# Optimization experiments

Hardware: AMD Instinct MI355X
Metric: run time of the kernel (lower is better)

Reference implementation:

```python
import jax, jax.numpy as jnp
import numpy as np

N_NODES = 100000
N_EDGES = 600000
VOCAB = 50000
EMBED_DIM = 128
HIDDEN_DIM = 128


def gcn_conv(h, W, b, src, dst, n_nodes):
    """PyG GCNConv: x' = D^{-1/2} (A+I) D^{-1/2} X W + b.
    src/dst already include self-loops."""
    hw = h @ W                                   # [N, out]
    deg = jnp.zeros((n_nodes,), hw.dtype).at[dst].add(1.0)   # in-degree incl. self-loop
    dinv = jax.lax.rsqrt(deg)                    # deg >= 1 thanks to self-loops
    norm = dinv[src] * dinv[dst]                 # [E+N]
    msgs = norm[:, None] * hw[src]               # gather [E+N, out]
    out = jnp.zeros_like(hw).at[dst].add(msgs)   # scatter-aggregate
    return out + b


def setup_inputs() -> dict:
    key = jax.random.key(0)
    ks = jax.random.split(key, 8)
    x = jax.random.randint(ks[0], (N_NODES,), 0, VOCAB, dtype=jnp.int64 if jax.config.jax_enable_x64 else jnp.int32)
    edge_index = jax.random.randint(ks[1], (2, N_EDGES), 0, N_NODES, dtype=jnp.int32)
    emb = jax.random.normal(ks[2], (VOCAB, EMBED_DIM), dtype=jnp.float32)
    # Glorot-style scale for GCN weights
    W1 = jax.random.normal(ks[3], (EMBED_DIM, HIDDEN_DIM), dtype=jnp.float32) * (1.0 / np.sqrt(EMBED_DIM))
    b1 = jnp.zeros((HIDDEN_DIM,), dtype=jnp.float32)
    W2 = jax.random.normal(ks[4], (HIDDEN_DIM, HIDDEN_DIM), dtype=jnp.float32) * (1.0 / np.sqrt(HIDDEN_DIM))
    b2 = jnp.zeros((HIDDEN_DIM,), dtype=jnp.float32)
    return {"x": x, "edge_index": edge_index, "emb": emb, "W1": W1, "b1": b1, "W2": W2, "b2": b2}


def reference(x, edge_index, emb, W1, b1, W2, b2):
    n = x.shape[0]
    loops = jnp.arange(n, dtype=edge_index.dtype)
    src = jnp.concatenate([edge_index[0], loops])  # add self-loops once
    dst = jnp.concatenate([edge_index[1], loops])
    h = emb[x]                                     # [N, embed_dim] embedding lookup
    h = jax.nn.relu(gcn_conv(h, W1, b1, src, dst, n))
    h = jax.nn.relu(gcn_conv(h, W2, b2, src, dst, n))
    return h
```

## Files before the change

kernel.cpp:

```cpp
#include <hip/hip_runtime.h>
#include <hip/hip_fp16.h>


#define NDIM 128
#define PAD_K 136
#define SCAN_IPT 4
#define SCAN_BLK 256
#define SCAN_IPB (SCAN_BLK * SCAN_IPT)

typedef __bf16 bf16x8 __attribute__((ext_vector_type(8)));
typedef float f32x4 __attribute__((ext_vector_type(4)));

__device__ __forceinline__ float bf2f(unsigned short u) {
    union { unsigned int i; float f; } c;
    c.i = (unsigned int)u << 16;
    return c.f;
}
__device__ __forceinline__ unsigned short f2bf(float f) {
    __bf16 b = (__bf16)f;
    return __builtin_bit_cast(unsigned short, b);
}
__device__ __forceinline__ unsigned short f2h(float f) {
    __half h = __float2half_rn(f);
    return __builtin_bit_cast(unsigned short, h);
}
__device__ __forceinline__ float h2f(unsigned short u) {
    return __half2float(__builtin_bit_cast(__half, u));
}
__device__ __forceinline__ void unpack8(uint4 q, float* f) {
    f[0] = bf2f((unsigned short)(q.x & 0xffff));
    f[1] = bf2f((unsigned short)(q.x >> 16));
    f[2] = bf2f((unsigned short)(q.y & 0xffff));
    f[3] = bf2f((unsigned short)(q.y >> 16));
    f[4] = bf2f((unsigned short)(q.z & 0xffff));
    f[5] = bf2f((unsigned short)(q.z >> 16));
    f[6] = bf2f((unsigned short)(q.w & 0xffff));
    f[7] = bf2f((unsigned short)(q.w >> 16));
}

__global__ void degree_count(const int* __restrict__ dst, int* __restrict__ cnt, int E) {
    const int stride = gridDim.x * blockDim.x;
    int e = blockIdx.x * blockDim.x + threadIdx.x;
#pragma unroll
    for (int k = 0; k < 4; ++k) {
        int ee = e + k * stride;
        if (ee < E) atomicAdd(&cnt[dst[ee]], 1);
    }
}

__global__ void scan_blocks(const int* __restrict__ in, int* __restrict__ out,
                            int* __restrict__ bsums, int n) {
    __shared__ int lds[SCAN_BLK];
    const int t = threadIdx.x;
    const int base = blockIdx.x * SCAN_IPB + t * SCAN_IPT;
    int v[SCAN_IPT];
    int s = 0;
#pragma unroll
    for (int k = 0; k < SCAN_IPT; ++k) { v[k] = (base + k < n) ? in[base + k] : 0; s += v[k]; }
    lds[t] = s;
    __syncthreads();
    for (int off = 1; off < SCAN_BLK; off <<= 1) {
        int x = (t >= off) ? lds[t - off] : 0;
        __syncthreads();
        lds[t] += x;
        __syncthreads();
    }
    if (t == SCAN_BLK - 1) bsums[blockIdx.x] = lds[t];
    int run = (t == 0) ? 0 : lds[t - 1];
#pragma unroll
    for (int k = 0; k < SCAN_IPT; ++k) {
        if (base + k < n) out[base + k] = run;
        run += v[k];
    }
}

__global__ void scan_partials(int* __restrict__ bsums, int nb) {
    __shared__ int lds[128];
    const int t = threadIdx.x;
    lds[t] = (t < nb) ? bsums[t] : 0;
    __syncthreads();
    for (int off = 1; off < 128; off <<= 1) {
        int x = (t >= off) ? lds[t - off] : 0;
        __syncthreads();
        lds[t] += x;
        __syncthreads();
    }
    if (t < nb) bsums[t] = (t == 0) ? 0 : lds[t - 1];
}

__global__ void add_offsets_dinv_wt(int* __restrict__ rp, const int* __restrict__ bsums,
                                    const int* __restrict__ cnt, float* __restrict__ dinv, int n,
                                    int nblkA,
                                    const float* __restrict__ W1, const float* __restrict__ W2,
                                    unsigned short* __restrict__ WT1,
                                    unsigned short* __restrict__ WT2) {
    if ((int)blockIdx.x < nblkA) {
        int i = blockIdx.x * blockDim.x + threadIdx.x;
        if (i < n) {
            rp[i] += bsums[i / SCAN_IPB];
            dinv[i] = rsqrtf((float)cnt[i] + 1.0f);
        }
    } else {
        int c = (blockIdx.x - nblkA) * blockDim.x + threadIdx.x;
        int cc = c & 16383;
        int j = cc >> 7, k = cc & 127;
        if (c < 16384) WT1[cc] = f2bf(W1[k * 128 + j]);
        else if (c < 32768) WT2[cc] = f2bf(W2[k * 128 + j]);
    }
}

__global__ void fill_edges(const int* __restrict__ src, const int* __restrict__ dst,
                           int* __restrict__ rp, const int* __restrict__ x,
                           const float* __restrict__ dinv, int2* __restrict__ ew, int E) {
    const int stride = gridDim.x * blockDim.x;
    const int e0 = blockIdx.x * blockDim.x + threadIdx.x;
    int s[4], d[4];
#pragma unroll
    for (int k = 0; k < 4; ++k) {
        int ee = e0 + k * stride;
        if (ee < E) { s[k] = src[ee]; d[k] = dst[ee]; } else { s[k] = -1; }
    }
    int xs[4];
    float ds[4];
#pragma unroll
    for (int k = 0; k < 4; ++k) {
        if (s[k] >= 0) { xs[k] = x[s[k]]; ds[k] = dinv[s[k]]; }
    }
#pragma unroll
    for (int k = 0; k < 4; ++k) {
        if (s[k] >= 0) {
            int p = atomicAdd(&rp[d[k]], 1);
            ew[p] = make_int2(s[k], (int)(((unsigned)f2h(ds[k]) << 16) | (unsigned)xs[k]));
        }
    }
}

template <int MODE, bool SCALE>
__global__ __launch_bounds__(256, 4)
void gemm_mfma(const void* __restrict__ Asrc, const unsigned short* __restrict__ WTb,
               const float* __restrict__ dinv, unsigned short* __restrict__ outb, int n) {
    __shared__ __bf16 sBT[128 * PAD_K];
    const int tid = threadIdx.x;
    const int rbase = blockIdx.x * 64;

    {
        const uint4* bsrc = (const uint4*)WTb;
#pragma unroll
        for (int i = 0; i < 8; ++i) {
            int c = tid + i * 256;
            int j = c >> 4, u = c & 15;
            *(uint4*)&sBT[j * PAD_K + u * 8] = bsrc[c];
        }
    }
    __syncthreads();

    const int wave = tid >> 6, lane = tid & 63;
    const int quad = lane >> 4, lrow = lane & 15;
    int arow = rbase + wave * 16 + lrow;
    if (arow >= n) arow = n - 1;

    f32x4 acc[8];
#pragma unroll
    for (int nt = 0; nt < 8; ++nt) acc[nt] = (f32x4)0.0f;

#pragma unroll
    for (int ks = 0; ks < 4; ++ks) {
        const int kb = ks * 32 + quad * 8;
        bf16x8 a;
        if (MODE == 0) {
            const float4* A4 = (const float4*)Asrc;
            float4 v0 = A4[(size_t)arow * 32 + (kb >> 2)];
            float4 v1 = A4[(size_t)arow * 32 + (kb >> 2) + 1];
            a = (bf16x8){(__bf16)v0.x, (__bf16)v0.y, (__bf16)v0.z, (__bf16)v0.w,
                         (__bf16)v1.x, (__bf16)v1.y, (__bf16)v1.z, (__bf16)v1.w};
        } else {
            a = *(const bf16x8*)((const unsigned short*)Asrc + (size_t)arow * 128 + kb);
        }
#pragma unroll
        for (int nt = 0; nt < 8; ++nt) {
            bf16x8 b = *(const bf16x8*)&sBT[(nt * 16 + lrow) * PAD_K + kb];
            acc[nt] = __builtin_amdgcn_mfma_f32_16x16x32_bf16(a, b, acc[nt], 0, 0, 0);
        }
    }

#pragma unroll
    for (int r = 0; r < 4; ++r) {
        int grow = rbase + wave * 16 + quad * 4 + r;
        if (grow < n) {
            float dsc = SCALE ? dinv[grow] : 1.0f;
            unsigned short* orow = outb + (size_t)grow * NDIM + lrow;
#pragma unroll
            for (int nt = 0; nt < 8; ++nt)
                orow[nt * 16] = f2bf(SCALE ? dsc * acc[nt][r] : acc[nt][r]);
        }
    }
}

__global__ void aggregate1(const unsigned short* __restrict__ tab, const int* __restrict__ x,
                           const int* __restrict__ rp, const int2* __restrict__ ew,
                           const float* __restrict__ dinv, const float* __restrict__ bias,
                           unsigned short* __restrict__ outb, int n, int half) {
    int t = blockIdx.x * blockDim.x + threadIdx.x;
    int g = t >> 4, u = t & 15;
    if (g >= half) return;
    const uint4* tab4 = (const uint4*)tab;
    const int i0 = g, i1 = g + half;
    const bool has1 = (i1 < n);
    float di0 = dinv[i0];
    float di1 = has1 ? dinv[i1] : 0.0f;
    float acc0[8], acc1[8];
    {
        float f[8];
        unpack8(tab4[(size_t)x[i0] * 16 + u], f);
#pragma unroll
        for (int k = 0; k < 8; ++k) acc0[k] = di0 * f[k];
    }
    if (has1) {
        float f[8];
        unpack8(tab4[(size_t)x[i1] * 16 + u], f);
#pragma unroll
        for (int k = 0; k < 8; ++k) acc1[k] = di1 * f[k];
    }
    int j0 = (i0 == 0) ? 0 : rp[i0 - 1];
    const int e0 = rp[i0];
    int j1 = has1 ? rp[i1 - 1] : 0;
    const int e1 = has1 ? rp[i1] : 0;

    while (j0 + 2 <= e0 && j1 + 2 <= e1) {
        int2 a0 = ew[j0], a1 = ew[j0 + 1], c0 = ew[j1], c1 = ew[j1 + 1];
        uint4 qa0 = tab4[(size_t)(a0.y & 0xffff) * 16 + u];
        uint4 qa1 = tab4[(size_t)(a1.y & 0xffff) * 16 + u];
        uint4 qc0 = tab4[(size_t)(c0.y & 0xffff) * 16 + u];
        uint4 qc1 = tab4[(size_t)(c1.y & 0xffff) * 16 + u];
        float fa0[8], fa1[8], fc0[8], fc1[8];
        unpack8(qa0, fa0); unpack8(qa1, fa1); unpack8(qc0, fc0); unpack8(qc1, fc1);
        float na0 = h2f((unsigned short)((unsigned)a0.y >> 16));
        float na1 = h2f((unsigned short)((unsigned)a1.y >> 16));
        float nc0 = h2f((unsigned short)((unsigned)c0.y >> 16));
        float nc1 = h2f((unsigned short)((unsigned)c1.y >> 16));
#pragma unroll
        for (int k = 0; k < 8; ++k) {
            acc0[k] += fmaf(na0, fa0[k], na1 * fa1[k]);
            acc1[k] += fmaf(nc0, fc0[k], nc1 * fc1[k]);
        }
        j0 += 2; j1 += 2;
    }
    for (; j0 + 2 <= e0; j0 += 2) {
        int2 a0 = ew[j0], a1 = ew[j0 + 1];
        uint4 qa0 = tab4[(size_t)(a0.y & 0xffff) * 16 + u];
        uint4 qa1 = tab4[(size_t)(a1.y & 0xffff) * 16 + u];
        float fa0[8], fa1[8];
        unpack8(qa0, fa0); unpack8(qa1, fa1);
        float na0 = h2f((unsigned short)((unsigned)a0.y >> 16));
        float na1 = h2f((unsigned short)((unsigned)a1.y >> 16));
#pragma unroll
        for (int k = 0; k < 8; ++k) acc0[k] += fmaf(na0, fa0[k], na1 * fa1[k]);
    }
    if (j0 < e0) {
        int2 a = ew[j0];
        uint4 q = tab4[(size_t)(a.y & 0xffff) * 16 + u];
        float f[8];
        unpack8(q, f);
        float nm = h2f((unsigned short)((unsigned)a.y >> 16));
#pragma unroll
        for (int k = 0; k < 8; ++k) acc0[k] = fmaf(nm, f[k], acc0[k]);
    }
    for (; j1 + 2 <= e1; j1 += 2) {
        int2 c0 = ew[j1], c1 = ew[j1 + 1];
        uint4 qc0 = tab4[(size_t)(c0.y & 0xffff) * 16 + u];
        uint4 qc1 = tab4[(size_t)(c1.y & 0xffff) * 16 + u];
        float fc0[8], fc1[8];
        unpack8(qc0, fc0); unpack8(qc1, fc1);
        float nc0 = h2f((unsigned short)((unsigned)c0.y >> 16));
        float nc1 = h2f((unsigned short)((unsigned)c1.y >> 16));
#pragma unroll
        for (int k = 0; k < 8; ++k) acc1[k] += fmaf(nc0, fc0[k], nc1 * fc1[k]);
    }
    if (j1 < e1) {
        int2 c = ew[j1];
        uint4 q = tab4[(size_t)(c.y & 0xffff) * 16 + u];
        float f[8];
        unpack8(q, f);
        float nm = h2f((unsigned short)((unsigned)c.y >> 16));
#pragma unroll
        for (int k = 0; k < 8; ++k) acc1[k] = fmaf(nm, f[k], acc1[k]);
    }

    const float4 b0 = ((const float4*)bias)[u * 2];
    const float4 b1 = ((const float4*)bias)[u * 2 + 1];
    {
        float r[8];
        r[0] = fmaxf(fmaf(di0, acc0[0], b0.x), 0.0f);
        r[1] = fmaxf(fmaf(di0, acc0[1], b0.y), 0.0f);
        r[2] = fmaxf(fmaf(di0, acc0[2], b0.z), 0.0f);
        r[3] = fmaxf(fmaf(di0, acc0[3], b0.w), 0.0f);
        r[4] = fmaxf(fmaf(di0, acc0[4], b1.x), 0.0f);
        r[5] = fmaxf(fmaf(di0, acc0[5], b1.y), 0.0f);
        r[6] = fmaxf(fmaf(di0, acc0[6], b1.z), 0.0f);
        r[7] = fmaxf(fmaf(di0, acc0[7], b1.w), 0.0f);
        uint4 o;
        o.x = (unsigned)f2bf(r[0]) | ((unsigned)f2bf(r[1]) << 16);
        o.y = (unsigned)f2bf(r[2]) | ((unsigned)f2bf(r[3]) << 16);
        o.z = (unsigned)f2bf(r[4]) | ((unsigned)f2bf(r[5]) << 16);
        o.w = (unsigned)f2bf(r[6]) | ((unsigned)f2bf(r[7]) << 16);
        ((uint4*)outb)[(size_t)i0 * 16 + u] = o;
    }
    if (has1) {
        float r[8];
        r[0] = fmaxf(fmaf(di1, acc1[0], b0.x), 0.0f);
        r[1] = fmaxf(fmaf(di1, acc1[1], b0.y), 0.0f);
        r[2] = fmaxf(fmaf(di1, acc1[2], b0.z), 0.0f);
        r[3] = fmaxf(fmaf(di1, acc1[3], b0.w), 0.0f);
        r[4] = fmaxf(fmaf(di1, acc1[4], b1.x), 0.0f);
        r[5] = fmaxf(fmaf(di1, acc1[5], b1.y), 0.0f);
        r[6] = fmaxf(fmaf(di1, acc1[6], b1.z), 0.0f);
        r[7] = fmaxf(fmaf(di1, acc1[7], b1.w), 0.0f);
        uint4 o;
        o.x = (unsigned)f2bf(r[0]) | ((unsigned)f2bf(r[1]) << 16);
        o.y = (unsigned)f2bf(r[2]) | ((unsigned)f2bf(r[3]) << 16);
        o.z = (unsigned)f2bf(r[4]) | ((unsigned)f2bf(r[5]) << 16);
        o.w = (unsigned)f2bf(r[6]) | ((unsigned)f2bf(r[7]) << 16);
        ((uint4*)outb)[(size_t)i1 * 16 + u] = o;
    }
}

__global__ void aggregate2(const unsigned short* __restrict__ vs, const int* __restrict__ rp,
                           const int2* __restrict__ ew, const float* __restrict__ dinv,
                           const float* __restrict__ bias, float* __restrict__ out,
                           int n, int half) {
    int t = blockIdx.x * blockDim.x + threadIdx.x;
    int g = t >> 4, u = t & 15;
    if (g >= half) return;
    const uint4* vs4 = (const uint4*)vs;
    const int i0 = g, i1 = g + half;
    const bool has1 = (i1 < n);
    float acc0[8], acc1[8];
    unpack8(vs4[(size_t)i0 * 16 + u], acc0);
    if (has1) unpack8(vs4[(size_t)i1 * 16 + u], acc1);
    int j0 = (i0 == 0) ? 0 : rp[i0 - 1];
    const int e0 = rp[i0];
    int j1 = has1 ? rp[i1 - 1] : 0;
    const int e1 = has1 ? rp[i1] : 0;

    while (j0 + 2 <= e0 && j1 + 2 <= e1) {
        int s00 = ew[j0].x, s01 = ew[j0 + 1].x, s10 = ew[j1].x, s11 = ew[j1 + 1].x;
        uint4 q00 = vs4[(size_t)s00 * 16 + u];
        uint4 q01 = vs4[(size_t)s01 * 16 + u];
        uint4 q10 = vs4[(size_t)s10 * 16 + u];
        uint4 q11 = vs4[(size_t)s11 * 16 + u];
        float f00[8], f01[8], f10[8], f11[8];
        unpack8(q00, f00); unpack8(q01, f01); unpack8(q10, f10); unpack8(q11, f11);
#pragma unroll
        for (int k = 0; k < 8; ++k) {
            acc0[k] += f00[k] + f01[k];
            acc1[k] += f10[k] + f11[k];
        }
        j0 += 2; j1 += 2;
    }
    for (; j0 + 2 <= e0; j0 += 2) {
        int s00 = ew[j0].x, s01 = ew[j0 + 1].x;
        uint4 q00 = vs4[(size_t)s00 * 16 + u];
        uint4 q01 = vs4[(size_t)s01 * 16 + u];
        float f00[8], f01[8];
        unpack8(q00, f00); unpack8(q01, f01);
#pragma unroll
        for (int k = 0; k < 8; ++k) acc0[k] += f00[k] + f01[k];
    }
    if (j0 < e0) {
        uint4 q = vs4[(size_t)ew[j0].x * 16 + u];
        float f[8];
        unpack8(q, f);
#pragma unroll
        for (int k = 0; k < 8; ++k) acc0[k] += f[k];
    }
    for (; j1 + 2 <= e1; j1 += 2) {
        int s10 = ew[j1].x, s11 = ew[j1 + 1].x;
        uint4 q10 = vs4[(size_t)s10 * 16 + u];
        uint4 q11 = vs4[(size_t)s11 * 16 + u];
        float f10[8], f11[8];
        unpack8(q10, f10); unpack8(q11, f11);
#pragma unroll
        for (int k = 0; k < 8; ++k) acc1[k] += f10[k] + f11[k];
    }
    if (j1 < e1) {
        uint4 q = vs4[(size_t)ew[j1].x * 16 + u];
        float f[8];
        unpack8(q, f);
#pragma unroll
        for (int k = 0; k < 8; ++k) acc1[k] += f[k];
    }

    const float4 b0 = ((const float4*)bias)[u * 2];
    const float4 b1 = ((const float4*)bias)[u * 2 + 1];
    {
        float di = dinv[i0];
        float4 r0, r1;
        r0.x = fmaxf(fmaf(di, acc0[0], b0.x), 0.0f);
        r0.y = fmaxf(fmaf(di, acc0[1], b0.y), 0.0f);
        r0.z = fmaxf(fmaf(di, acc0[2], b0.z), 0.0f);
        r0.w = fmaxf(fmaf(di, acc0[3], b0.w), 0.0f);
        r1.x = fmaxf(fmaf(di, acc0[4], b1.x), 0.0f);
        r1.y = fmaxf(fmaf(di, acc0[5], b1.y), 0.0f);
        r1.z = fmaxf(fmaf(di, acc0[6], b1.z), 0.0f);
        r1.w = fmaxf(fmaf(di, acc0[7], b1.w), 0.0f);
        ((float4*)out)[(size_t)i0 * 32 + u * 2] = r0;
        ((float4*)out)[(size_t)i0 * 32 + u * 2 + 1] = r1;
    }
    if (has1) {
        float di = dinv[i1];
        float4 r0, r1;
        r0.x = fmaxf(fmaf(di, acc1[0], b0.x), 0.0f);
        r0.y = fmaxf(fmaf(di, acc1[1], b0.y), 0.0f);
        r0.z = fmaxf(fmaf(di, acc1[2], b0.z), 0.0f);
        r0.w = fmaxf(fmaf(di, acc1[3], b0.w), 0.0f);
        r1.x = fmaxf(fmaf(di, acc1[4], b1.x), 0.0f);
        r1.y = fmaxf(fmaf(di, acc1[5], b1.y), 0.0f);
        r1.z = fmaxf(fmaf(di, acc1[6], b1.z), 0.0f);
        r1.w = fmaxf(fmaf(di, acc1[7], b1.w), 0.0f);
        ((float4*)out)[(size_t)i1 * 32 + u * 2] = r0;
        ((float4*)out)[(size_t)i1 * 32 + u * 2 + 1] = r1;
    }
}

extern "C" void kernel_launch(void* const* d_in, const int* in_sizes, int n_in,
                              void* d_out, int out_size, void* d_ws, size_t ws_size,
                              hipStream_t stream) {
    const int* x = (const int*)d_in[0];
    const int* edge_index = (const int*)d_in[1];
    const float* emb = (const float*)d_in[2];
    const float* W1 = (const float*)d_in[3];
    const float* b1 = (const float*)d_in[4];
    const float* W2 = (const float*)d_in[5];
    const float* b2 = (const float*)d_in[6];
    float* out = (float*)d_out;

    const int N = in_sizes[0];
    const int E = in_sizes[1] / 2;
    const int V = in_sizes[2] / NDIM;
    const int* src = edge_index;
    const int* dst = edge_index + E;

    char* p = (char*)d_ws;
    auto alloc = [&](size_t bytes) {
        char* q = p;
        p += (bytes + 511) & ~(size_t)511;
        return q;
    };
    int* cnt = (int*)alloc((size_t)N * sizeof(int));
    int* rp = (int*)alloc((size_t)N * sizeof(int));
    float* dinv = (float*)alloc((size_t)N * sizeof(float));
    int* bsums = (int*)alloc(128 * sizeof(int));
    int2* ew = (int2*)alloc((size_t)E * sizeof(int2));
    unsigned short* WT1 = (unsigned short*)alloc(16384 * sizeof(unsigned short));
    unsigned short* WT2 = (unsigned short*)alloc(16384 * sizeof(unsigned short));
    unsigned short* embW1 = (unsigned short*)alloc((size_t)V * NDIM * sizeof(unsigned short));
    unsigned short* h1b = (unsigned short*)alloc((size_t)N * NDIM * sizeof(unsigned short));
    unsigned short* vs2 = (unsigned short*)alloc((size_t)N * NDIM * sizeof(unsigned short));
    (void)ws_size;

    const int NB = (N + SCAN_IPB - 1) / SCAN_IPB;
    const int nblkA = (N + 255) / 256;
    const int half = (N + 1) / 2;

    hipMemsetAsync(cnt, 0, (size_t)N * sizeof(int), stream);
    degree_count<<<(E / 4 + 255) / 256, 256, 0, stream>>>(dst, cnt, E);
    scan_blocks<<<NB, SCAN_BLK, 0, stream>>>(cnt, rp, bsums, N);
    scan_partials<<<1, 128, 0, stream>>>(bsums, NB);
    add_offsets_dinv_wt<<<nblkA + 128, 256, 0, stream>>>(rp, bsums, cnt, dinv, N, nblkA,
                                                         W1, W2, WT1, WT2);
    fill_edges<<<(E / 4 + 255) / 256, 256, 0, stream>>>(src, dst, rp, x, dinv, ew, E);

    const int agg_blocks = (int)(((size_t)half * 16 + 255) / 256);

    gemm_mfma<0, false><<<(V + 63) / 64, 256, 0, stream>>>(emb, WT1, nullptr, embW1, V);
    aggregate1<<<agg_blocks, 256, 0, stream>>>(embW1, x, rp, ew, dinv, b1, h1b, N, half);
    gemm_mfma<1, true><<<(N + 63) / 64, 256, 0, stream>>>(h1b, WT2, dinv, vs2, N);
    aggregate2<<<agg_blocks, 256, 0, stream>>>(vs2, rp, ew, dinv, b2, out, N, half);
}
```

Measured before the change: 251.8 us.

## Merge embedding GEMM and CSR edge fill into one launch

The embedding-table GEMM and the edge fill that builds the CSR are combined into a single heterogeneous kernel. Block index decides whether a block runs the MFMA GEMM or the fill. This lets the two independent stages run concurrently and removes one launch. Degree counting and the fill now process 2 edges per thread instead of 4, giving more blocks with less work each. The fill blocks carry the GEMM's shared-memory allocation and launch bounds, which may limit their occupancy.

```diff
diff --git a/kernel.cpp b/kernel.cpp
--- a/kernel.cpp
+++ b/kernel.cpp
@@ -42,7 +42,7 @@
     const int stride = gridDim.x * blockDim.x;
     int e = blockIdx.x * blockDim.x + threadIdx.x;
 #pragma unroll
-    for (int k = 0; k < 4; ++k) {
+    for (int k = 0; k < 2; ++k) {
         int ee = e + k * stride;
         if (ee < E) atomicAdd(&cnt[dst[ee]], 1);
     }
@@ -109,36 +109,83 @@
     }
 }
 
-__global__ void fill_edges(const int* __restrict__ src, const int* __restrict__ dst,
-                           int* __restrict__ rp, const int* __restrict__ x,
-                           const float* __restrict__ dinv, int2* __restrict__ ew, int E) {
-    const int stride = gridDim.x * blockDim.x;
-    const int e0 = blockIdx.x * blockDim.x + threadIdx.x;
-    int s[4], d[4];
-#pragma unroll
-    for (int k = 0; k < 4; ++k) {
-        int ee = e0 + k * stride;
-        if (ee < E) { s[k] = src[ee]; d[k] = dst[ee]; } else { s[k] = -1; }
-    }
-    int xs[4];
-    float ds[4];
-#pragma unroll
-    for (int k = 0; k < 4; ++k) {
-        if (s[k] >= 0) { xs[k] = x[s[k]]; ds[k] = dinv[s[k]]; }
-    }
-#pragma unroll
-    for (int k = 0; k < 4; ++k) {
-        if (s[k] >= 0) {
-            int p = atomicAdd(&rp[d[k]], 1);
-            ew[p] = make_int2(s[k], (int)(((unsigned)f2h(ds[k]) << 16) | (unsigned)xs[k]));
-        }
-    }
-}
-
-template <int MODE, bool SCALE>
 __global__ __launch_bounds__(256, 4)
-void gemm_mfma(const void* __restrict__ Asrc, const unsigned short* __restrict__ WTb,
-               const float* __restrict__ dinv, unsigned short* __restrict__ outb, int n) {
+void gemm1_fill(const float* __restrict__ emb, const unsigned short* __restrict__ WT1,
+                unsigned short* __restrict__ embW1, int V, int gemmBlocks,
+                const int* __restrict__ src, const int* __restrict__ dst,
+                int* __restrict__ rp, const int* __restrict__ x,
+                const float* __restrict__ dinv, int2* __restrict__ ew, int E,
+                int fillBlocks) {
+    __shared__ __bf16 sBT[128 * PAD_K];
+    const int tid = threadIdx.x;
+
+    if ((int)blockIdx.x < gemmBlocks) {
+        const int rbase = blockIdx.x * 64;
+        {
+            const uint4* bsrc = (const uint4*)WT1;
+#pragma unroll
+            for (int i = 0; i < 8; ++i) {
+                int c = tid + i * 256;
+                int j = c >> 4, u = c & 15;
+                *(uint4*)&sBT[j * PAD_K + u * 8] = bsrc[c];
+            }
+        }
+        __syncthreads();
+
+        const int wave = tid >> 6, lane = tid & 63;
+        const int quad = lane >> 4, lrow = lane & 15;
+        int arow = rbase + wave * 16 + lrow;
+        if (arow >= V) arow = V - 1;
+
+        f32x4 acc[8];
+#pragma unroll
+        for (int nt = 0; nt < 8; ++nt) acc[nt] = (f32x4)0.0f;
+
+#pragma unroll
+        for (int ks = 0; ks < 4; ++ks) {
+            const int kb = ks * 32 + quad * 8;
+            const float4* A4 = (const float4*)emb;
+            float4 v0 = A4[(size_t)arow * 32 + (kb >> 2)];
+            float4 v1 = A4[(size_t)arow * 32 + (kb >> 2) + 1];
+            bf16x8 a = (bf16x8){(__bf16)v0.x, (__bf16)v0.y, (__bf16)v0.z, (__bf16)v0.w,
+                                (__bf16)v1.x, (__bf16)v1.y, (__bf16)v1.z, (__bf16)v1.w};
+#pragma unroll
+            for (int nt = 0; nt < 8; ++nt) {
+                bf16x8 b = *(const bf16x8*)&sBT[(nt * 16 + lrow) * PAD_K + kb];
+                acc[nt] = __builtin_amdgcn_mfma_f32_16x16x32_bf16(a, b, acc[nt], 0, 0, 0);
+            }
+        }
+
+#pragma unroll
+        for (int r = 0; r < 4; ++r) {
+            int grow = rbase + wave * 16 + quad * 4 + r;
+            if (grow < V) {
+                unsigned short* orow = embW1 + (size_t)grow * NDIM + lrow;
+#pragma unroll
+                for (int nt = 0; nt < 8; ++nt)
+                    orow[nt * 16] = f2bf(acc[nt][r]);
+            }
+        }
+    } else {
+        const int bid = blockIdx.x - gemmBlocks;
+        const int stride = fillBlocks * 256;
+        int e = bid * 256 + tid;
+#pragma unroll
+        for (int k = 0; k < 2; ++k, e += stride) {
+            if (e < E) {
+                int d = dst[e], s = src[e];
+                int xs = x[s];
+                float ds = dinv[s];
+                int p = atomicAdd(&rp[d], 1);
+                ew[p] = make_int2(s, (int)(((unsigned)f2h(ds) << 16) | (unsigned)xs));
+            }
+        }
+    }
+}
+
+__global__ __launch_bounds__(256, 4)
+void gemm_mfma_b(const unsigned short* __restrict__ Asrc, const unsigned short* __restrict__ WTb,
+                 const float* __restrict__ dinv, unsigned short* __restrict__ outb, int n) {
     __shared__ __bf16 sBT[128 * PAD_K];
     const int tid = threadIdx.x;
     const int rbase = blockIdx.x * 64;
@@ -166,16 +213,7 @@
 #pragma unroll
     for (int ks = 0; ks < 4; ++ks) {
         const int kb = ks * 32 + quad * 8;
-        bf16x8 a;
-        if (MODE == 0) {
-            const float4* A4 = (const float4*)Asrc;
-            float4 v0 = A4[(size_t)arow * 32 + (kb >> 2)];
-            float4 v1 = A4[(size_t)arow * 32 + (kb >> 2) + 1];
-            a = (bf16x8){(__bf16)v0.x, (__bf16)v0.y, (__bf16)v0.z, (__bf16)v0.w,
-                         (__bf16)v1.x, (__bf16)v1.y, (__bf16)v1.z, (__bf16)v1.w};
-        } else {
-            a = *(const bf16x8*)((const unsigned short*)Asrc + (size_t)arow * 128 + kb);
-        }
+        bf16x8 a = *(const bf16x8*)(Asrc + (size_t)arow * 128 + kb);
 #pragma unroll
         for (int nt = 0; nt < 8; ++nt) {
             bf16x8 b = *(const bf16x8*)&sBT[(nt * 16 + lrow) * PAD_K + kb];
@@ -187,11 +225,11 @@
     for (int r = 0; r < 4; ++r) {
         int grow = rbase + wave * 16 + quad * 4 + r;
         if (grow < n) {
-            float dsc = SCALE ? dinv[grow] : 1.0f;
+            float dsc = dinv[grow];
             unsigned short* orow = outb + (size_t)grow * NDIM + lrow;
 #pragma unroll
             for (int nt = 0; nt < 8; ++nt)
-                orow[nt * 16] = f2bf(SCALE ? dsc * acc[nt][r] : acc[nt][r]);
+                orow[nt * 16] = f2bf(dsc * acc[nt][r]);
         }
     }
 }
@@ -461,19 +499,22 @@
     const int NB = (N + SCAN_IPB - 1) / SCAN_IPB;
     const int nblkA = (N + 255) / 256;
     const int half = (N + 1) / 2;
+    const int gemmBlocks = (V + 63) / 64;
+    const int fillBlocks = (E / 2 + 255) / 256;
 
     hipMemsetAsync(cnt, 0, (size_t)N * sizeof(int), stream);
-    degree_count<<<(E / 4 + 255) / 256, 256, 0, stream>>>(dst, cnt, E);
+    degree_count<<<(E / 2 + 255) / 256, 256, 0, stream>>>(dst, cnt, E);
     scan_blocks<<<NB, SCAN_BLK, 0, stream>>>(cnt, rp, bsums, N);
     scan_partials<<<1, 128, 0, stream>>>(bsums, NB);
     add_offsets_dinv_wt<<<nblkA + 128, 256, 0, stream>>>(rp, bsums, cnt, dinv, N, nblkA,
                                                          W1, W2, WT1, WT2);
-    fill_edges<<<(E / 4 + 255) / 256, 256, 0, stream>>>(src, dst, rp, x, dinv, ew, E);
+
+    gemm1_fill<<<gemmBlocks + fillBlocks, 256, 0, stream>>>(
+        emb, WT1, embW1, V, gemmBlocks, src, dst, rp, x, dinv, ew, E, fillBlocks);
 
     const int agg_blocks = (int)(((size_t)half * 16 + 255) / 256);
 
-    gemm_mfma<0, false><<<(V + 63) / 64, 256, 0, stream>>>(emb, WT1, nullptr, embW1, V);
     aggregate1<<<agg_blocks, 256, 0, stream>>>(embW1, x, rp, ew, dinv, b1, h1b, N, half);
-    gemm_mfma<1, true><<<(N + 63) / 64, 256, 0, stream>>>(h1b, WT2, dinv, vs2, N);
+    gemm_mfma_b<<<(N + 63) / 64, 256, 0, stream>>>(h1b, WT2, dinv, vs2, N);
     aggregate2<<<agg_blocks, 256, 0, stream>>>(vs2, rp, ew, dinv, b2, out, N, half);
 }
```

New measurement: 242.1 us. 3.8% less time.
